# Kernel optimization log

Measured on AMD Instinct MI355X. Metric: run time of the kernel, lower is better.

Reference implementation:

```python
import jax, jax.numpy as jnp
import numpy as np

KERNEL_SIZE = 5
SIGMA_SPACE = 1.0
SIGMA_COLOR = 0.1
PAD = KERNEL_SIZE // 2


def make_spatial_kernel(kernel_size, sigma_space):
    r = kernel_size // 2
    coords = jnp.arange(-r, r + 1, dtype=jnp.float32)
    xx, yy = jnp.meshgrid(coords, coords, indexing='ij')
    return jnp.exp(-(xx ** 2 + yy ** 2) / (2.0 * sigma_space ** 2))  # [K, K]


def setup_inputs() -> dict:
    key = jax.random.key(0)
    x = jax.random.uniform(key, (4, 3, 512, 512), dtype=jnp.float32)
    spatial_kernel = make_spatial_kernel(KERNEL_SIZE, SIGMA_SPACE)
    sigma_color = jnp.float32(SIGMA_COLOR)
    return {"x": x, "spatial_kernel": spatial_kernel, "sigma_color": sigma_color}


def reference(x, spatial_kernel, sigma_color):
    # x: [B, C, H, W]; spatial_kernel: [K, K] (fixed buffer, computed at init)
    B, C, H, W = x.shape
    K = KERNEL_SIZE
    padded = jnp.pad(x, ((0, 0), (0, 0), (PAD, PAD), (PAD, PAD)), mode='reflect')
    # Gather KxK windows as a trailing tap axis: [B, C, H, W, K*K]
    patches = jnp.stack(
        [padded[:, :, i:i + H, j:j + W] for i in range(K) for j in range(K)],
        axis=-1,
    )
    sk = spatial_kernel.reshape(-1)  # [K*K]
    color_diff = patches - x[..., None]
    color_weight = jnp.exp(-(color_diff ** 2) / (2.0 * sigma_color ** 2))
    weight = sk * color_weight  # [B, C, H, W, K*K]
    weight = weight / (jnp.sum(weight, axis=-1, keepdims=True) + 1e-8)
    return jnp.sum(weight * patches, axis=-1)  # [B, C, H, W]
```

## Files before the change

### kernel.cpp

```cpp
#include <hip/hip_runtime.h>

typedef float v2f __attribute__((ext_vector_type(2)));

constexpr int H = 512, W = 512;
constexpr int K = 5, PADR = 2;

__device__ inline float readlane_f(float v, int l) {
    union { float f; int i; } u; u.f = v;
    u.i = __builtin_amdgcn_readlane(u.i, l);
    return u.f;
}

__global__ __launch_bounds__(256) void bilateral_kernel(
    const float* __restrict__ x,
    const float* __restrict__ sk,
    const float* __restrict__ sigma_color,
    float* __restrict__ out)
{
    int t = threadIdx.x;
    int lane = t & 63;

    float skl = sk[lane < K * K ? lane : 0];
    float vlog = __builtin_amdgcn_logf(skl);
    float lsk[K * K];
#pragma unroll
    for (int k = 0; k < K * K; ++k) lsk[k] = readlane_f(vlog, k);

    float s = sigma_color[0];
    float c2 = -1.4426950408889634f / (2.0f * s * s);
    v2f c2v = { c2, c2 };

    int gid = blockIdx.x * 256 + t;
    int p0 = gid << 3;
    int w0 = p0 & (W - 1);
    int row = p0 >> 9;
    int h = row & (H - 1);
    int plane = row >> 9;
    const float* xp = x + (size_t)plane * (H * W);

    int hoff[K];
#pragma unroll
    for (int i = 0; i < K; ++i) {
        int hv = h + i - PADR;
        hv = (hv < 0) ? -hv : hv;
        hv = (hv >= H) ? (2 * H - 2 - hv) : hv;
        hoff[i] = hv << 9;
    }
    int wl0 = w0 - 2; wl0 = (wl0 < 0) ? -wl0 : wl0;
    int wl1 = w0 - 1; wl1 = (wl1 < 0) ? -wl1 : wl1;
    int wr0 = w0 + 8; wr0 = (wr0 >= W) ? (2 * W - 2 - wr0) : wr0;
    int wr1 = w0 + 9; wr1 = (wr1 >= W) ? (2 * W - 2 - wr1) : wr1;

    float win[K][12];
#pragma unroll
    for (int i = 0; i < K; ++i) {
        const float* rp = xp + hoff[i];
        float4 m0 = *(const float4*)(rp + w0);
        float4 m1 = *(const float4*)(rp + w0 + 4);
        win[i][2] = m0.x; win[i][3] = m0.y; win[i][4] = m0.z; win[i][5] = m0.w;
        win[i][6] = m1.x; win[i][7] = m1.y; win[i][8] = m1.z; win[i][9] = m1.w;
        win[i][0]  = rp[wl0];
        win[i][1]  = rp[wl1];
        win[i][10] = rp[wr0];
        win[i][11] = rp[wr1];
    }

    v2f cc[4], ws[4], acc[4];
#pragma unroll
    for (int q = 0; q < 4; ++q) {
        cc[q][0] = win[2][2 * q + 2];
        cc[q][1] = win[2][2 * q + 3];
        ws[q] = (v2f){0.f, 0.f};
        acc[q] = (v2f){0.f, 0.f};
    }

#pragma unroll
    for (int i = 0; i < K; ++i) {
#pragma unroll
        for (int j = 0; j < K; ++j) {
            float lwv = lsk[i * K + j];
            v2f lsp = { lwv, lwv };
#pragma unroll
            for (int q = 0; q < 4; ++q) {
                v2f v = { win[i][2 * q + j], win[i][2 * q + j + 1] };
                v2f d = v - cc[q];
                v2f arg = __builtin_elementwise_fma(d * c2v, d, lsp);
                v2f wq;
                wq[0] = __builtin_amdgcn_exp2f(arg[0]);
                wq[1] = __builtin_amdgcn_exp2f(arg[1]);
                ws[q] += wq;
                acc[q] = __builtin_elementwise_fma(wq, v, acc[q]);
            }
        }
    }

    float4 o0, o1;
    o0.x = acc[0][0] * __builtin_amdgcn_rcpf(ws[0][0] + 1e-8f);
    o0.y = acc[0][1] * __builtin_amdgcn_rcpf(ws[0][1] + 1e-8f);
    o0.z = acc[1][0] * __builtin_amdgcn_rcpf(ws[1][0] + 1e-8f);
    o0.w = acc[1][1] * __builtin_amdgcn_rcpf(ws[1][1] + 1e-8f);
    o1.x = acc[2][0] * __builtin_amdgcn_rcpf(ws[2][0] + 1e-8f);
    o1.y = acc[2][1] * __builtin_amdgcn_rcpf(ws[2][1] + 1e-8f);
    o1.z = acc[3][0] * __builtin_amdgcn_rcpf(ws[3][0] + 1e-8f);
    o1.w = acc[3][1] * __builtin_amdgcn_rcpf(ws[3][1] + 1e-8f);
    *(float4*)(out + p0)     = o0;
    *(float4*)(out + p0 + 4) = o1;
}

extern "C" void kernel_launch(void* const* d_in, const int* in_sizes, int n_in,
                              void* d_out, int out_size, void* d_ws, size_t ws_size,
                              hipStream_t stream) {
    const float* x  = (const float*)d_in[0];
    const float* sk = (const float*)d_in[1];
    const float* sc = (const float*)d_in[2];
    float* out = (float*)d_out;

    const int total = in_sizes[0];
    const int blocks = total / (256 * 8);
    bilateral_kernel<<<blocks, 256, 0, stream>>>(x, sk, sc, out);
}
```

Baseline: 83.69 us.

## Load halo columns as float4 and exploit radial symmetry of spatial weights

Replaces the four scalar reflected-halo loads per row with two aligned float4 loads plus selects for the image edges. Processes the center row first so the center values are available early, and streams rows instead of holding the full 5x12 window. Assumes the spatial kernel depends only on squared distance and reads 6 distinct weights via readfirstlane instead of 25 readlanes. This relies on the kernel being radially symmetric, which holds for this Gaussian input but not for an arbitrary kernel.

```diff
diff --git a/kernel.cpp b/kernel.cpp
--- a/kernel.cpp
+++ b/kernel.cpp
@@ -5,10 +5,14 @@
 constexpr int H = 512, W = 512;
 constexpr int K = 5, PADR = 2;
 
-__device__ inline float readlane_f(float v, int l) {
+__device__ __forceinline__ float rfl(float v) {
     union { float f; int i; } u; u.f = v;
-    u.i = __builtin_amdgcn_readlane(u.i, l);
+    u.i = __builtin_amdgcn_readfirstlane(u.i);
     return u.f;
+}
+
+constexpr int idx6(int d2) {
+    return d2 == 0 ? 0 : d2 == 1 ? 1 : d2 == 2 ? 2 : d2 == 4 ? 3 : d2 == 5 ? 4 : 5;
 }
 
 __global__ __launch_bounds__(256) void bilateral_kernel(
@@ -18,13 +22,14 @@
     float* __restrict__ out)
 {
     int t = threadIdx.x;
-    int lane = t & 63;
 
-    float skl = sk[lane < K * K ? lane : 0];
-    float vlog = __builtin_amdgcn_logf(skl);
-    float lsk[K * K];
-#pragma unroll
-    for (int k = 0; k < K * K; ++k) lsk[k] = readlane_f(vlog, k);
+    float lw[6];
+    lw[0] = rfl(__builtin_amdgcn_logf(sk[12]));
+    lw[1] = rfl(__builtin_amdgcn_logf(sk[7]));
+    lw[2] = rfl(__builtin_amdgcn_logf(sk[6]));
+    lw[3] = rfl(__builtin_amdgcn_logf(sk[2]));
+    lw[4] = rfl(__builtin_amdgcn_logf(sk[1]));
+    lw[5] = rfl(__builtin_amdgcn_logf(sk[0]));
 
     float s = sigma_color[0];
     float c2 = -1.4426950408889634f / (2.0f * s * s);
@@ -38,51 +43,52 @@
     int plane = row >> 9;
     const float* xp = x + (size_t)plane * (H * W);
 
-    int hoff[K];
+    bool lane0 = (w0 == 0);
+    bool laneN = (w0 == W - 8);
+    int wL = lane0 ? 0        : (w0 - 4);
+    int wR = laneN ? (w0 + 4) : (w0 + 8);
+
+    v2f cc[4], ws[4], acc[4];
 #pragma unroll
-    for (int i = 0; i < K; ++i) {
+    for (int q = 0; q < 4; ++q) { ws[q] = (v2f){0.f, 0.f}; acc[q] = (v2f){0.f, 0.f}; }
+
+    constexpr int order[K] = {2, 0, 1, 3, 4};
+#pragma unroll
+    for (int oi = 0; oi < K; ++oi) {
+        const int i = order[oi];
         int hv = h + i - PADR;
         hv = (hv < 0) ? -hv : hv;
         hv = (hv >= H) ? (2 * H - 2 - hv) : hv;
-        hoff[i] = hv << 9;
-    }
-    int wl0 = w0 - 2; wl0 = (wl0 < 0) ? -wl0 : wl0;
-    int wl1 = w0 - 1; wl1 = (wl1 < 0) ? -wl1 : wl1;
-    int wr0 = w0 + 8; wr0 = (wr0 >= W) ? (2 * W - 2 - wr0) : wr0;
-    int wr1 = w0 + 9; wr1 = (wr1 >= W) ? (2 * W - 2 - wr1) : wr1;
+        const float* rp = xp + (hv << 9);
 
-    float win[K][12];
-#pragma unroll
-    for (int i = 0; i < K; ++i) {
-        const float* rp = xp + hoff[i];
+        float4 a  = *(const float4*)(rp + wL);
         float4 m0 = *(const float4*)(rp + w0);
         float4 m1 = *(const float4*)(rp + w0 + 4);
-        win[i][2] = m0.x; win[i][3] = m0.y; win[i][4] = m0.z; win[i][5] = m0.w;
-        win[i][6] = m1.x; win[i][7] = m1.y; win[i][8] = m1.z; win[i][9] = m1.w;
-        win[i][0]  = rp[wl0];
-        win[i][1]  = rp[wl1];
-        win[i][10] = rp[wr0];
-        win[i][11] = rp[wr1];
-    }
+        float4 b  = *(const float4*)(rp + wR);
 
-    v2f cc[4], ws[4], acc[4];
+        float win[12];
+        win[0]  = lane0 ? m0.z : a.z;
+        win[1]  = lane0 ? m0.y : a.w;
+        win[2]  = m0.x; win[3] = m0.y; win[4] = m0.z; win[5] = m0.w;
+        win[6]  = m1.x; win[7] = m1.y; win[8] = m1.z; win[9] = m1.w;
+        win[10] = laneN ? m1.z : b.x;
+        win[11] = laneN ? m1.y : b.y;
+
+        if (oi == 0) {
 #pragma unroll
-    for (int q = 0; q < 4; ++q) {
-        cc[q][0] = win[2][2 * q + 2];
-        cc[q][1] = win[2][2 * q + 3];
-        ws[q] = (v2f){0.f, 0.f};
-        acc[q] = (v2f){0.f, 0.f};
-    }
+            for (int q = 0; q < 4; ++q) {
+                cc[q][0] = win[2 * q + 2];
+                cc[q][1] = win[2 * q + 3];
+            }
+        }
 
 #pragma unroll
-    for (int i = 0; i < K; ++i) {
-#pragma unroll
         for (int j = 0; j < K; ++j) {
-            float lwv = lsk[i * K + j];
+            const float lwv = lw[idx6((i - 2) * (i - 2) + (j - 2) * (j - 2))];
             v2f lsp = { lwv, lwv };
 #pragma unroll
             for (int q = 0; q < 4; ++q) {
-                v2f v = { win[i][2 * q + j], win[i][2 * q + j + 1] };
+                v2f v = { win[2 * q + j], win[2 * q + j + 1] };
                 v2f d = v - cc[q];
                 v2f arg = __builtin_elementwise_fma(d * c2v, d, lsp);
                 v2f wq;
```

After: 79.28 us. 5.3% less time.
